# Optimization experiments

Measured on AMD Instinct MI355X. Metric: run time of the kernel, lower is better.

Reference implementation:

```python
import jax, jax.numpy as jnp
import numpy as np

N = 100000
E = 1280000
C = 64
MID = 256
OUT = 64
BN_EPS = 1e-5


def setup_inputs() -> dict:
    key = jax.random.key(0)
    ks = jax.random.split(key, 8)
    x = jax.random.normal(ks[0], (N, C), dtype=jnp.float32)
    edge_index = jax.random.randint(ks[1], (2, E), 0, N, dtype=jnp.int64)
    edge_attr = jax.random.normal(ks[2], (E, 1), dtype=jnp.float32)
    batch = jnp.zeros((N,), dtype=jnp.int64)
    # MLP params: Lin(2C->MID), BatchNorm1d(MID), Lin(MID->OUT)
    W1 = jax.random.normal(ks[3], (2 * C, MID), dtype=jnp.float32) / np.sqrt(2 * C)
    b1 = jnp.zeros((MID,), dtype=jnp.float32)
    gamma = jnp.ones((MID,), dtype=jnp.float32)
    beta = jnp.zeros((MID,), dtype=jnp.float32)
    W2 = jax.random.normal(ks[4], (MID, OUT), dtype=jnp.float32) / np.sqrt(MID)
    b2 = jnp.zeros((OUT,), dtype=jnp.float32)
    return {"x": x, "edge_index": edge_index, "edge_attr": edge_attr, "batch": batch,
            "W1": W1, "b1": b1, "gamma": gamma, "beta": beta, "W2": W2, "b2": b2}


def reference(x, edge_index, edge_attr, batch, W1, b1, gamma, beta, W2, b2):
    n = x.shape[0]
    row, col = edge_index[0], edge_index[1]
    xc = x[col]                                  # [E, C] irregular gather
    feat = jnp.concatenate([xc, xc * edge_attr], axis=1)  # [E, 2C]
    sums = jax.ops.segment_sum(feat, row, num_segments=n)  # [N, 2C]
    cnt = jax.ops.segment_sum(jnp.ones((feat.shape[0],), feat.dtype), row, num_segments=n)
    agg = sums / jnp.maximum(cnt, 1.0)[:, None]  # scatter_mean
    # MLP: Lin -> ReLU -> BatchNorm1d (training stats) -> Lin
    h = jax.nn.relu(agg @ W1 + b1)
    mu = jnp.mean(h, axis=0)
    var = jnp.var(h, axis=0)                     # biased var, as torch BN uses
    h = (h - mu) * jax.lax.rsqrt(var + BN_EPS) * gamma + beta
    return h @ W2 + b2
```

## Files before the change

kernel.cpp:

```cpp
#include <hip/hip_runtime.h>
#include <hip/hip_bf16.h>

#define MIDF 256
#define OUTF 64
#define CF 64
#define TWO_C 128
#define BN_EPS 1e-5f
#define BCAP 2048

typedef __attribute__((ext_vector_type(8))) short bf16x8;
typedef __attribute__((ext_vector_type(4))) float f32x4;

__device__ __forceinline__ ushort f2bf(float f) {
  union { float f; unsigned u; } v; v.f = f;
  return (ushort)((v.u + 0x7fffu + ((v.u >> 16) & 1u)) >> 16);
}
__device__ __forceinline__ float bf2f(unsigned u16) {
  union { unsigned u; float f; } v; v.u = u16 << 16;
  return v.f;
}

__global__ __launch_bounds__(256) void k_xcast(const float4* __restrict__ xp,
    uint4* __restrict__ xb, int* __restrict__ gcur, float* __restrict__ bnacc, int n8) {
  int i = blockIdx.x * blockDim.x + threadIdx.x;
  if (i < 1024) gcur[i] = i * BCAP;
  else if (i < 1536) bnacc[i - 1024] = 0.f;
  int st = gridDim.x * blockDim.x;
  for (; i < n8; i += st) {
    float4 a = xp[2 * i], b = xp[2 * i + 1];
    uint4 o;
    o.x = (unsigned)f2bf(a.x) | ((unsigned)f2bf(a.y) << 16);
    o.y = (unsigned)f2bf(a.z) | ((unsigned)f2bf(a.w) << 16);
    o.z = (unsigned)f2bf(b.x) | ((unsigned)f2bf(b.y) << 16);
    o.w = (unsigned)f2bf(b.z) | ((unsigned)f2bf(b.w) << 16);
    xb[i] = o;
  }
}

__global__ __launch_bounds__(256) void k_bscatter(const int* __restrict__ ei,
    const float* __restrict__ ea, int* __restrict__ gcur,
    uint2* __restrict__ ebt, int E) {
  __shared__ int lh[1024];
  __shared__ int lb[1024];
  int tid = threadIdx.x;
  int c0 = blockIdx.x * 4096;
  for (int b = tid; b < 1024; b += 256) lh[b] = 0;
  __syncthreads();
  int rows[16];
#pragma unroll
  for (int j = 0; j < 16; ++j) {
    int e = c0 + j * 256 + tid;
    int r = (e < E) ? ei[e] : -1;
    rows[j] = r;
    if (r >= 0) atomicAdd(&lh[r >> 7], 1);
  }
  __syncthreads();
  for (int b = tid; b < 1024; b += 256) {
    int c = lh[b];
    lb[b] = (c > 0) ? atomicAdd(&gcur[b], c) : 0;
  }
  __syncthreads();
#pragma unroll
  for (int j = 0; j < 16; ++j) {
    int r = rows[j];
    if (r >= 0) {
      int e = c0 + j * 256 + tid;
      int pos = atomicAdd(&lb[r >> 7], 1);
      ebt[pos] = make_uint2((unsigned)ei[E + e] | ((unsigned)(r & 127) << 20),
                            __float_as_uint(ea[e]));
    }
  }
}

__global__ __launch_bounds__(256) void k_bsort(const uint2* __restrict__ ebt,
    const int* __restrict__ gcur, uint2* __restrict__ eb,
    int* __restrict__ starts, int* __restrict__ deg, int n) {
  __shared__ int hist[128];
  __shared__ int cursor[128];
  __shared__ int wtot;
  int tid = threadIdx.x, lane = tid & 63;
  int b = blockIdx.x;
  int base = b * BCAP;
  int e = gcur[b];
  if (tid < 128) hist[tid] = 0;
  __syncthreads();
  for (int i = base + tid; i < e; i += 256)
    atomicAdd(&hist[ebt[i].x >> 20], 1);
  __syncthreads();
  if (tid < 128) {
    int v = hist[tid];
    int sc = v;
#pragma unroll
    for (int d = 1; d < 64; d <<= 1) {
      int t = __shfl_up(sc, d);
      if (lane >= d) sc += t;
    }
    if (tid == 63) wtot = sc;
    cursor[tid] = sc - v;
  }
  __syncthreads();
  if (tid < 128) {
    int st = base + cursor[tid] + ((tid >= 64) ? wtot : 0);
    cursor[tid] = st;
    int r = (b << 7) + tid;
    if (r < n) { starts[r] = st; deg[r] = hist[tid]; }
  }
  __syncthreads();
  for (int i = base + tid; i < e; i += 256) {
    uint2 rec = ebt[i];
    int pos = atomicAdd(&cursor[rec.x >> 20], 1);
    eb[pos] = make_uint2(rec.x & 0xFFFFF, rec.y);
  }
}

__global__ void k_agg(const ushort* __restrict__ xb, const uint2* __restrict__ eb,
                      const int* __restrict__ starts, const int* __restrict__ deg,
                      ushort* __restrict__ agg, int n) {
  int lane = threadIdx.x & 63;
  int q4 = lane >> 4, l16 = lane & 15;
  int wave = (blockIdx.x * blockDim.x + threadIdx.x) >> 6;
  int nw = (gridDim.x * blockDim.x) >> 6;
  for (int v = wave; v < n; v += nw) {
    int s = starts[v], d = deg[v];
    int e = s + d;
    float s0 = 0.f, s1 = 0.f, s2 = 0.f, s3 = 0.f;
    float t0 = 0.f, t1 = 0.f, t2 = 0.f, t3 = 0.f;
    int i = s + q4;
    for (; i + 4 < e; i += 8) {
      uint2 pa = eb[i], pb = eb[i + 4];
      uint2 xa = *(const uint2*)(xb + (size_t)pa.x * CF + 4 * l16);
      uint2 xc = *(const uint2*)(xb + (size_t)pb.x * CF + 4 * l16);
      float wa = __uint_as_float(pa.y), wb = __uint_as_float(pb.y);
      float a0 = bf2f(xa.x & 0xffff), a1 = bf2f(xa.x >> 16);
      float a2 = bf2f(xa.y & 0xffff), a3 = bf2f(xa.y >> 16);
      float b0 = bf2f(xc.x & 0xffff), b1 = bf2f(xc.x >> 16);
      float b2 = bf2f(xc.y & 0xffff), b3 = bf2f(xc.y >> 16);
      s0 += a0 + b0; s1 += a1 + b1; s2 += a2 + b2; s3 += a3 + b3;
      t0 += a0 * wa + b0 * wb; t1 += a1 * wa + b1 * wb;
      t2 += a2 * wa + b2 * wb; t3 += a3 * wa + b3 * wb;
    }
    if (i < e) {
      uint2 p = eb[i];
      uint2 xv = *(const uint2*)(xb + (size_t)p.x * CF + 4 * l16);
      float w = __uint_as_float(p.y);
      float a0 = bf2f(xv.x & 0xffff), a1 = bf2f(xv.x >> 16);
      float a2 = bf2f(xv.y & 0xffff), a3 = bf2f(xv.y >> 16);
      s0 += a0; s1 += a1; s2 += a2; s3 += a3;
      t0 += a0 * w; t1 += a1 * w; t2 += a2 * w; t3 += a3 * w;
    }
    s0 += __shfl_xor(s0, 16); s1 += __shfl_xor(s1, 16);
    s2 += __shfl_xor(s2, 16); s3 += __shfl_xor(s3, 16);
    t0 += __shfl_xor(t0, 16); t1 += __shfl_xor(t1, 16);
    t2 += __shfl_xor(t2, 16); t3 += __shfl_xor(t3, 16);
    s0 += __shfl_xor(s0, 32); s1 += __shfl_xor(s1, 32);
    s2 += __shfl_xor(s2, 32); s3 += __shfl_xor(s3, 32);
    t0 += __shfl_xor(t0, 32); t1 += __shfl_xor(t1, 32);
    t2 += __shfl_xor(t2, 32); t3 += __shfl_xor(t3, 32);
    float inv = 1.0f / fmaxf((float)d, 1.0f);
    if (q4 == 0) {
      uint2 o;
      o.x = (unsigned)f2bf(s0 * inv) | ((unsigned)f2bf(s1 * inv) << 16);
      o.y = (unsigned)f2bf(s2 * inv) | ((unsigned)f2bf(s3 * inv) << 16);
      *(uint2*)(agg + (size_t)v * TWO_C + 4 * l16) = o;
      uint2 p2;
      p2.x = (unsigned)f2bf(t0 * inv) | ((unsigned)f2bf(t1 * inv) << 16);
      p2.y = (unsigned)f2bf(t2 * inv) | ((unsigned)f2bf(t3 * inv) << 16);
      *(uint2*)(agg + (size_t)v * TWO_C + CF + 4 * l16) = p2;
    }
  }
}

__global__ __launch_bounds__(256, 3) void k_gemm1(const ushort* __restrict__ agg,
    const float* __restrict__ W1, const float* __restrict__ b1,
    ushort* __restrict__ h, float* __restrict__ bnacc, int n, int ntiles) {
  int tid = threadIdx.x, w = tid >> 6, lane = tid & 63;
  int q = lane >> 4, l16 = lane & 15;
  int cg = blockIdx.x & 3;
  int colbase = cg * 64;
  bf16x8 Bf[4][4];
#pragma unroll
  for (int ct = 0; ct < 4; ++ct)
#pragma unroll
    for (int ks = 0; ks < 4; ++ks) {
      int c = colbase + ct * 16 + l16;
      int k0 = ks * 32 + q * 8;
#pragma unroll
      for (int j = 0; j < 8; ++j)
        Bf[ct][ks][j] = (short)f2bf(W1[(size_t)(k0 + j) * MIDF + c]);
    }
  float bias[4];
#pragma unroll
  for (int ct = 0; ct < 4; ++ct) bias[ct] = b1[colbase + ct * 16 + l16];
  __shared__ ushort tile[64 * 72];
  int c_stat = tid & 63, rb = tid >> 6;
  float s_sum = 0.f, s_sq = 0.f;
  int nb = gridDim.x >> 2;
  for (int t = blockIdx.x >> 2; t < ntiles; t += nb) {
    int r0 = t * 64;
    int myrow = r0 + w * 16 + l16;
    bf16x8 Af[4];
#pragma unroll
    for (int ks = 0; ks < 4; ++ks) {
      bf16x8 av;
#pragma unroll
      for (int j = 0; j < 8; ++j) av[j] = 0;
      if (myrow < n) av = *(const bf16x8*)(agg + (size_t)myrow * TWO_C + ks * 32 + q * 8);
      Af[ks] = av;
    }
    f32x4 acc[4];
#pragma unroll
    for (int ct = 0; ct < 4; ++ct) acc[ct] = (f32x4){0.f, 0.f, 0.f, 0.f};
#pragma unroll
    for (int ks = 0; ks < 4; ++ks)
#pragma unroll
      for (int ct = 0; ct < 4; ++ct)
        acc[ct] = __builtin_amdgcn_mfma_f32_16x16x32_bf16(Af[ks], Bf[ct][ks], acc[ct], 0, 0, 0);
    __syncthreads();
#pragma unroll
    for (int ct = 0; ct < 4; ++ct)
#pragma unroll
      for (int r = 0; r < 4; ++r) {
        float vv = fmaxf(acc[ct][r] + bias[ct], 0.f);
        tile[(w * 16 + q * 4 + r) * 72 + ct * 16 + l16] = f2bf(vv);
      }
    __syncthreads();
    int row = tid >> 2, co = (tid & 3) * 16;
    int gr = r0 + row;
    if (gr < n) {
      const uint4* src = (const uint4*)(tile + row * 72 + co);
      uint4* dst = (uint4*)(h + (size_t)gr * MIDF + colbase + co);
      dst[0] = src[0];
      dst[1] = src[1];
    }
#pragma unroll 4
    for (int r = 0; r < 16; ++r) {
      int rr = rb * 16 + r;
      if (r0 + rr < n) {
        float vv = bf2f(tile[rr * 72 + c_stat]);
        s_sum += vv;
        s_sq += vv * vv;
      }
    }
  }
  __syncthreads();
  float* red = (float*)tile;
  red[rb * 64 + c_stat] = s_sum;
  red[256 + rb * 64 + c_stat] = s_sq;
  __syncthreads();
  if (tid < 128) {
    int c = tid & 63, isq = tid >> 6;
    int base = isq * 256;
    float v = red[base + c] + red[base + 64 + c] + red[base + 128 + c] + red[base + 192 + c];
    atomicAdd(&bnacc[isq * MIDF + colbase + c], v);
  }
}

__global__ __launch_bounds__(256) void k_final(const float* __restrict__ bnacc,
    const float* __restrict__ gamma, const float* __restrict__ beta,
    const float* __restrict__ W2, const float* __restrict__ b2,
    float* __restrict__ W2p, float* __restrict__ b2p, float invN) {
  __shared__ float scb[MIDF], shb[MIDF], red[256];
  int tid = threadIdx.x;
  float s = bnacc[tid];
  float q = bnacc[MIDF + tid];
  float mu = s * invN;
  float var = q * invN - mu * mu;
  float sc = gamma[tid] * rsqrtf(var + BN_EPS);
  scb[tid] = sc;
  shb[tid] = beta[tid] - mu * sc;
  __syncthreads();
  float sp = 0.f;
  for (int i = tid; i < MIDF * OUTF; i += 256) {
    int k = i >> 6;
    float wv = W2[i];
    W2p[i] = scb[k] * wv;
    sp += shb[k] * wv;
  }
  red[tid] = sp;
  __syncthreads();
  if (tid < 64)
    b2p[tid] = b2[tid] + red[tid] + red[64 + tid] + red[128 + tid] + red[192 + tid];
}

__global__ __launch_bounds__(256, 2) void k_gemm2(const ushort* __restrict__ h,
    const float* __restrict__ W2p, const float* __restrict__ b2p,
    float* __restrict__ out, int n, int ntiles) {
  int tid = threadIdx.x, w = tid >> 6, lane = tid & 63;
  int q = lane >> 4, l16 = lane & 15;
  bf16x8 Bf[4][8];
#pragma unroll
  for (int ct = 0; ct < 4; ++ct)
#pragma unroll
    for (int ks = 0; ks < 8; ++ks) {
      int c = ct * 16 + l16;
      int k0 = ks * 32 + q * 8;
#pragma unroll
      for (int j = 0; j < 8; ++j)
        Bf[ct][ks][j] = (short)f2bf(W2p[(size_t)(k0 + j) * OUTF + c]);
    }
  float bias[4];
#pragma unroll
  for (int ct = 0; ct < 4; ++ct) bias[ct] = b2p[ct * 16 + l16];
  __shared__ float tile[64 * 68];
  for (int t = blockIdx.x; t < ntiles; t += gridDim.x) {
    int r0 = t * 64;
    int myrow = r0 + w * 16 + l16;
    f32x4 acc[4];
#pragma unroll
    for (int ct = 0; ct < 4; ++ct) acc[ct] = (f32x4){0.f, 0.f, 0.f, 0.f};
#pragma unroll
    for (int ks = 0; ks < 8; ++ks) {
      bf16x8 av;
#pragma unroll
      for (int j = 0; j < 8; ++j) av[j] = 0;
      if (myrow < n) av = *(const bf16x8*)(h + (size_t)myrow * MIDF + ks * 32 + q * 8);
#pragma unroll
      for (int ct = 0; ct < 4; ++ct)
        acc[ct] = __builtin_amdgcn_mfma_f32_16x16x32_bf16(av, Bf[ct][ks], acc[ct], 0, 0, 0);
    }
    __syncthreads();
#pragma unroll
    for (int ct = 0; ct < 4; ++ct)
#pragma unroll
      for (int r = 0; r < 4; ++r)
        tile[(w * 16 + q * 4 + r) * 68 + ct * 16 + l16] = acc[ct][r] + bias[ct];
    __syncthreads();
    int row = tid >> 2, co = (tid & 3) * 16;
    int gr = r0 + row;
    if (gr < n) {
      const float4* src = (const float4*)(tile + row * 68 + co);
      float4* dst = (float4*)(out + (size_t)gr * OUTF + co);
      dst[0] = src[0];
      dst[1] = src[1];
      dst[2] = src[2];
      dst[3] = src[3];
    }
  }
}

extern "C" void kernel_launch(void* const* d_in, const int* in_sizes, int n_in,
                              void* d_out, int out_size, void* d_ws, size_t ws_size,
                              hipStream_t stream) {
  const float* x     = (const float*)d_in[0];
  const int*   ei    = (const int*)d_in[1];
  const float* ea    = (const float*)d_in[2];
  const float* W1    = (const float*)d_in[4];
  const float* b1    = (const float*)d_in[5];
  const float* gamma = (const float*)d_in[6];
  const float* beta  = (const float*)d_in[7];
  const float* W2    = (const float*)d_in[8];
  const float* b2    = (const float*)d_in[9];
  float* out = (float*)d_out;
  int E = in_sizes[2];
  int n = in_sizes[3];
  int NB = (n + 127) >> 7;

  char* ws = (char*)d_ws;
  ushort* agg = (ushort*)ws;
  ushort* h   = agg + (size_t)n * TWO_C;
  ushort* xb  = h + (size_t)n * MIDF;
  float* W2p  = (float*)(xb + (size_t)n * CF);
  float* b2p  = W2p + MIDF * OUTF;
  int* gcur   = (int*)(b2p + 64);
  float* bnacc= (float*)(gcur + 1024);
  int* starts = (int*)(bnacc + 512);
  int* deg    = starts + n;
  uint2* ebt  = (uint2*)h;
  uint2* eb   = ebt + 1024 * BCAP;

  hipLaunchKernelGGL(k_xcast, dim3(512), dim3(256), 0, stream,
                     (const float4*)x, (uint4*)xb, gcur, bnacc, n * CF / 8);
  int nchunks = (E + 4095) / 4096;
  hipLaunchKernelGGL(k_bscatter, dim3(nchunks), dim3(256), 0, stream, ei, ea, gcur, ebt, E);
  hipLaunchKernelGGL(k_bsort, dim3(NB), dim3(256), 0, stream, ebt, gcur, eb, starts, deg, n);
  hipLaunchKernelGGL(k_agg, dim3(4096), dim3(256), 0, stream, xb, eb, starts, deg, agg, n);
  int nt = (n + 63) / 64;
  hipLaunchKernelGGL(k_gemm1, dim3(1024), dim3(256), 0, stream, agg, W1, b1, h, bnacc, n, nt);
  hipLaunchKernelGGL(k_final, dim3(1), dim3(256), 0, stream, bnacc, gamma, beta,
                     W2, b2, W2p, b2p, 1.0f / (float)n);
  hipLaunchKernelGGL(k_gemm2, dim3(512), dim3(256), 0, stream, h, W2p, b2p, out, n, nt);
}
```

Measured before the change: 256.4 us.

## Fuse bucket sort into aggregation using shared-memory sorted records per 64-row bucket

Merges the per-bucket counting sort and the mean-aggregation kernel so that each block sorts its bucket's edge records into LDS and aggregates straight from there. This drops the global write and re-read of the sorted edge array and the starts/deg arrays, and removes one launch. Buckets shrink from 128 to 64 rows with capacity 1024. The gemm1 grid also changes from 1024 to 768 blocks. The main risks are bucket overflow for high-degree inputs and the fixed work of 8 rows per wave, which may hurt load balance.

```diff
diff --git a/kernel.cpp b/kernel.cpp
--- a/kernel.cpp
+++ b/kernel.cpp
@@ -6,7 +6,8 @@
 #define CF 64
 #define TWO_C 128
 #define BN_EPS 1e-5f
-#define BCAP 2048
+#define BCAP 1024
+#define NBMAX 1600
 
 typedef __attribute__((ext_vector_type(8))) short bf16x8;
 typedef __attribute__((ext_vector_type(4))) float f32x4;
@@ -21,10 +22,11 @@
 }
 
 __global__ __launch_bounds__(256) void k_xcast(const float4* __restrict__ xp,
-    uint4* __restrict__ xb, int* __restrict__ gcur, float* __restrict__ bnacc, int n8) {
+    uint4* __restrict__ xb, int* __restrict__ gcur, float* __restrict__ bnacc,
+    int n8, int NB) {
   int i = blockIdx.x * blockDim.x + threadIdx.x;
-  if (i < 1024) gcur[i] = i * BCAP;
-  else if (i < 1536) bnacc[i - 1024] = 0.f;
+  if (i < NB) gcur[i] = i * BCAP;
+  else if (i < NB + 512) bnacc[i - NB] = 0.f;
   int st = gridDim.x * blockDim.x;
   for (; i < n8; i += st) {
     float4 a = xp[2 * i], b = xp[2 * i + 1];
@@ -39,12 +41,12 @@
 
 __global__ __launch_bounds__(256) void k_bscatter(const int* __restrict__ ei,
     const float* __restrict__ ea, int* __restrict__ gcur,
-    uint2* __restrict__ ebt, int E) {
-  __shared__ int lh[1024];
-  __shared__ int lb[1024];
+    uint2* __restrict__ ebt, int E, int NB) {
+  __shared__ int lh[NBMAX];
+  __shared__ int lb[NBMAX];
   int tid = threadIdx.x;
   int c0 = blockIdx.x * 4096;
-  for (int b = tid; b < 1024; b += 256) lh[b] = 0;
+  for (int b = tid; b < NB; b += 256) lh[b] = 0;
   __syncthreads();
   int rows[16];
 #pragma unroll
@@ -52,10 +54,10 @@
     int e = c0 + j * 256 + tid;
     int r = (e < E) ? ei[e] : -1;
     rows[j] = r;
-    if (r >= 0) atomicAdd(&lh[r >> 7], 1);
-  }
-  __syncthreads();
-  for (int b = tid; b < 1024; b += 256) {
+    if (r >= 0) atomicAdd(&lh[r >> 6], 1);
+  }
+  __syncthreads();
+  for (int b = tid; b < NB; b += 256) {
     int c = lh[b];
     lb[b] = (c > 0) ? atomicAdd(&gcur[b], c) : 0;
   }
@@ -65,69 +67,59 @@
     int r = rows[j];
     if (r >= 0) {
       int e = c0 + j * 256 + tid;
-      int pos = atomicAdd(&lb[r >> 7], 1);
-      ebt[pos] = make_uint2((unsigned)ei[E + e] | ((unsigned)(r & 127) << 20),
+      int pos = atomicAdd(&lb[r >> 6], 1);
+      ebt[pos] = make_uint2((unsigned)ei[E + e] | ((unsigned)(r & 63) << 20),
                             __float_as_uint(ea[e]));
     }
   }
 }
 
-__global__ __launch_bounds__(256) void k_bsort(const uint2* __restrict__ ebt,
-    const int* __restrict__ gcur, uint2* __restrict__ eb,
-    int* __restrict__ starts, int* __restrict__ deg, int n) {
-  __shared__ int hist[128];
-  __shared__ int cursor[128];
-  __shared__ int wtot;
-  int tid = threadIdx.x, lane = tid & 63;
+__global__ __launch_bounds__(512, 4) void k_sortagg(const ushort* __restrict__ xb,
+    const uint2* __restrict__ ebt, const int* __restrict__ gcur,
+    ushort* __restrict__ agg, int n) {
+  __shared__ uint2 recs[BCAP];
+  __shared__ int hist[64], cbase[64], cursor[64];
+  int tid = threadIdx.x;
   int b = blockIdx.x;
   int base = b * BCAP;
-  int e = gcur[b];
-  if (tid < 128) hist[tid] = 0;
-  __syncthreads();
-  for (int i = base + tid; i < e; i += 256)
-    atomicAdd(&hist[ebt[i].x >> 20], 1);
-  __syncthreads();
-  if (tid < 128) {
+  int cnt = gcur[b] - base;
+  if (tid < 64) hist[tid] = 0;
+  __syncthreads();
+  for (int i = tid; i < cnt; i += 512)
+    atomicAdd(&hist[(ebt[base + i].x >> 20) & 63], 1);
+  __syncthreads();
+  if (tid < 64) {
     int v = hist[tid];
     int sc = v;
 #pragma unroll
     for (int d = 1; d < 64; d <<= 1) {
       int t = __shfl_up(sc, d);
-      if (lane >= d) sc += t;
-    }
-    if (tid == 63) wtot = sc;
+      if (tid >= d) sc += t;
+    }
+    cbase[tid] = sc - v;
     cursor[tid] = sc - v;
   }
   __syncthreads();
-  if (tid < 128) {
-    int st = base + cursor[tid] + ((tid >= 64) ? wtot : 0);
-    cursor[tid] = st;
-    int r = (b << 7) + tid;
-    if (r < n) { starts[r] = st; deg[r] = hist[tid]; }
-  }
-  __syncthreads();
-  for (int i = base + tid; i < e; i += 256) {
-    uint2 rec = ebt[i];
-    int pos = atomicAdd(&cursor[rec.x >> 20], 1);
-    eb[pos] = make_uint2(rec.x & 0xFFFFF, rec.y);
-  }
-}
-
-__global__ void k_agg(const ushort* __restrict__ xb, const uint2* __restrict__ eb,
-                      const int* __restrict__ starts, const int* __restrict__ deg,
-                      ushort* __restrict__ agg, int n) {
-  int lane = threadIdx.x & 63;
+  for (int i = tid; i < cnt; i += 512) {
+    uint2 rec = ebt[base + i];
+    int pos = atomicAdd(&cursor[(rec.x >> 20) & 63], 1);
+    recs[pos] = make_uint2(rec.x & 0xFFFFF, rec.y);
+  }
+  __syncthreads();
+  int w = tid >> 6, lane = tid & 63;
   int q4 = lane >> 4, l16 = lane & 15;
-  int wave = (blockIdx.x * blockDim.x + threadIdx.x) >> 6;
-  int nw = (gridDim.x * blockDim.x) >> 6;
-  for (int v = wave; v < n; v += nw) {
-    int s = starts[v], d = deg[v];
+#pragma unroll
+  for (int j = 0; j < 8; ++j) {
+    int rl = w * 8 + j;
+    int v = (b << 6) + rl;
+    if (v >= n) continue;
+    int s = cbase[rl], d = hist[rl];
     int e = s + d;
     float s0 = 0.f, s1 = 0.f, s2 = 0.f, s3 = 0.f;
     float t0 = 0.f, t1 = 0.f, t2 = 0.f, t3 = 0.f;
     int i = s + q4;
     for (; i + 4 < e; i += 8) {
-      uint2 pa = eb[i], pb = eb[i + 4];
+      uint2 pa = recs[i], pb = recs[i + 4];
       uint2 xa = *(const uint2*)(xb + (size_t)pa.x * CF + 4 * l16);
       uint2 xc = *(const uint2*)(xb + (size_t)pb.x * CF + 4 * l16);
       float wa = __uint_as_float(pa.y), wb = __uint_as_float(pb.y);
@@ -140,13 +132,13 @@
       t2 += a2 * wa + b2 * wb; t3 += a3 * wa + b3 * wb;
     }
     if (i < e) {
-      uint2 p = eb[i];
+      uint2 p = recs[i];
       uint2 xv = *(const uint2*)(xb + (size_t)p.x * CF + 4 * l16);
-      float w = __uint_as_float(p.y);
+      float wt = __uint_as_float(p.y);
       float a0 = bf2f(xv.x & 0xffff), a1 = bf2f(xv.x >> 16);
       float a2 = bf2f(xv.y & 0xffff), a3 = bf2f(xv.y >> 16);
       s0 += a0; s1 += a1; s2 += a2; s3 += a3;
-      t0 += a0 * w; t1 += a1 * w; t2 += a2 * w; t3 += a3 * w;
+      t0 += a0 * wt; t1 += a1 * wt; t2 += a2 * wt; t3 += a3 * wt;
     }
     s0 += __shfl_xor(s0, 16); s1 += __shfl_xor(s1, 16);
     s2 += __shfl_xor(s2, 16); s3 += __shfl_xor(s3, 16);
@@ -353,7 +345,7 @@
   float* out = (float*)d_out;
   int E = in_sizes[2];
   int n = in_sizes[3];
-  int NB = (n + 127) >> 7;
+  int NB = (n + 63) >> 6;
 
   char* ws = (char*)d_ws;
   ushort* agg = (ushort*)ws;
@@ -362,20 +354,16 @@
   float* W2p  = (float*)(xb + (size_t)n * CF);
   float* b2p  = W2p + MIDF * OUTF;
   int* gcur   = (int*)(b2p + 64);
-  float* bnacc= (float*)(gcur + 1024);
-  int* starts = (int*)(bnacc + 512);
-  int* deg    = starts + n;
+  float* bnacc= (float*)(gcur + NBMAX);
   uint2* ebt  = (uint2*)h;
-  uint2* eb   = ebt + 1024 * BCAP;
 
   hipLaunchKernelGGL(k_xcast, dim3(512), dim3(256), 0, stream,
-                     (const float4*)x, (uint4*)xb, gcur, bnacc, n * CF / 8);
+                     (const float4*)x, (uint4*)xb, gcur, bnacc, n * CF / 8, NB);
   int nchunks = (E + 4095) / 4096;
-  hipLaunchKernelGGL(k_bscatter, dim3(nchunks), dim3(256), 0, stream, ei, ea, gcur, ebt, E);
-  hipLaunchKernelGGL(k_bsort, dim3(NB), dim3(256), 0, stream, ebt, gcur, eb, starts, deg, n);
-  hipLaunchKernelGGL(k_agg, dim3(4096), dim3(256), 0, stream, xb, eb, starts, deg, agg, n);
+  hipLaunchKernelGGL(k_bscatter, dim3(nchunks), dim3(256), 0, stream, ei, ea, gcur, ebt, E, NB);
+  hipLaunchKernelGGL(k_sortagg, dim3(NB), dim3(512), 0, stream, xb, ebt, gcur, agg, n);
   int nt = (n + 63) / 64;
-  hipLaunchKernelGGL(k_gemm1, dim3(1024), dim3(256), 0, stream, agg, W1, b1, h, bnacc, n, nt);
+  hipLaunchKernelGGL(k_gemm1, dim3(768), dim3(256), 0, stream, agg, W1, b1, h, bnacc, n, nt);
   hipLaunchKernelGGL(k_final, dim3(1), dim3(256), 0, stream, bnacc, gamma, beta,
                      W2, b2, W2p, b2p, 1.0f / (float)n);
   hipLaunchKernelGGL(k_gemm2, dim3(512), dim3(256), 0, stream, h, W2p, b2p, out, n, nt);
```

Result: faster. 243.9 us (-4.9%).
